# Performance work log

Measured on AMD Instinct MI355X. Metric: run time of the kernel, lower is better.

## Reference

```python
import jax, jax.numpy as jnp
import numpy as np

B, S, D, H = 4, 1024, 1024, 16
HD = D // H


def setup_inputs() -> dict:
    key = jax.random.key(0)
    ks = jax.random.split(key, 8)
    q = jax.random.normal(ks[0], (B, S, D), jnp.float32)
    q_mask = jnp.ones((B, S), dtype=bool)
    kv_mask = jax.random.randint(ks[1], (B, S), 0, 2).astype(bool)
    edge_weights = jax.random.uniform(ks[2], (B, S, S), jnp.float32)
    w_init = 0.02
    wq = jax.random.normal(ks[3], (D, D), jnp.float32) * w_init
    wk = jax.random.normal(ks[4], (D, D), jnp.float32) * w_init
    wv = jax.random.normal(ks[5], (D, D), jnp.float32) * w_init
    wo = jax.random.normal(ks[6], (D, D), jnp.float32) * w_init
    bo = jnp.zeros((D,), jnp.float32)
    return {"q": q, "q_mask": q_mask, "kv_mask": kv_mask,
            "edge_weights": edge_weights, "wq": wq, "wk": wk, "wv": wv,
            "wo": wo, "bo": bo}


def _pass_with_mask(x, w, mask, b=None):
    # Linear applied everywhere, padded rows zeroed (matches pass_with_mask)
    y = x @ w.T
    if b is not None:
        y = y + b
    return jnp.where(mask[..., None], y, 0.0)


def reference(q, q_mask, kv_mask, edge_weights, wq, wk, wv, wo, bo):
    b = q.shape[0]
    # merge_masks: padding mask outer product (recv x send)
    full_mask = (q_mask[:, :, None] & kv_mask[:, None, :])[:, None]  # [b,1,s,s]
    # projections (self attention: k = v = q)
    qh = _pass_with_mask(q, wq, q_mask).reshape(b, S, H, HD).transpose(0, 2, 1, 3)
    kh = _pass_with_mask(q, wk, kv_mask).reshape(b, S, H, HD).transpose(0, 2, 1, 3)
    vh = _pass_with_mask(q, wv, kv_mask).reshape(b, S, H, HD).transpose(0, 2, 1, 3)
    # NOTE: faithful to source, scaled by sqrt(model_dim), not sqrt(head_dim)
    scores = jnp.einsum("bhqd,bhkd->bhqk", qh, kh) / np.sqrt(D).astype(np.float32)
    scores = scores * edge_weights[:, None]          # mul_weights=True
    scores = jnp.where(full_mask, scores, -jnp.inf)
    scores = jax.nn.softmax(scores, axis=-1)
    scores = jnp.where(full_mask, scores, 0.0)       # re-zero masked entries
    out = jnp.einsum("bhqk,bhkd->bhqd", scores, vh)
    out = out.transpose(0, 2, 1, 3).reshape(b, S, D)
    return _pass_with_mask(out, wo, q_mask, bo)
```

## Files before the change

kernel.cpp:

```cpp
#include <hip/hip_runtime.h>

typedef unsigned short u16;
typedef unsigned int u32;
typedef __bf16 b16x8 __attribute__((ext_vector_type(8)));
typedef u16 u16x8 __attribute__((ext_vector_type(8)));
typedef float f32x4 __attribute__((ext_vector_type(4)));
typedef float f32x16 __attribute__((ext_vector_type(16)));
typedef u32 u32x2 __attribute__((ext_vector_type(2)));

#define DEV __device__ __forceinline__
#define INF __builtin_inff()
#define MFMA16(a, b, c) __builtin_amdgcn_mfma_f32_16x16x32_bf16((a), (b), (c), 0, 0, 0)
#define MFMA32(a, b, c) __builtin_amdgcn_mfma_f32_32x32x16_bf16((a), (b), (c), 0, 0, 0)
#define EXP2F(x) __builtin_amdgcn_exp2f(x)

DEV u16 f2b(float f) {
  union { float f; unsigned u; } x; x.f = f;
  unsigned r = x.u + 0x7fffu + ((x.u >> 16) & 1u);
  return (u16)(r >> 16);
}

DEV u32 pk2(float a, float b) {
  __bf16 lo = (__bf16)a, hi = (__bf16)b;
  u16 ul, uh;
  __builtin_memcpy(&ul, &lo, 2);
  __builtin_memcpy(&uh, &hi, 2);
  return (u32)ul | ((u32)uh << 16);
}

DEV float b2f(u16 v) {
  union { u32 u; float f; } x; x.u = (u32)v << 16; return x.f;
}

DEV void gl_lds16(const u16* g, u16* l) {
  __builtin_amdgcn_global_load_lds((const __attribute__((address_space(1))) void*)g,
                                   (__attribute__((address_space(3))) void*)l, 16, 0, 0);
}

__global__ __launch_bounds__(256) void cvt_all(const float* __restrict__ q,
                                               const float* __restrict__ wq,
                                               const float* __restrict__ wk,
                                               const float* __restrict__ wv,
                                               const float* __restrict__ wo,
                                               u16* __restrict__ xb, u16* __restrict__ wqb,
                                               u16* __restrict__ wkb, u16* __restrict__ wvb,
                                               u16* __restrict__ wob) {
  const int blk = blockIdx.x;
  const float* src; u16* dst; float scale = 1.f; int base;
  if (blk < 4096)      { src = q;  dst = xb;  base = blk; }
  else if (blk < 5120) { src = wq; dst = wqb; base = blk - 4096; scale = 0.045084441f; }
  else if (blk < 6144) { src = wk; dst = wkb; base = blk - 5120; }
  else if (blk < 7168) { src = wv; dst = wvb; base = blk - 6144; }
  else                 { src = wo; dst = wob; base = blk - 7168; }
  const int i = base * 256 + threadIdx.x;
  float4 v = reinterpret_cast<const float4*>(src)[i];
  ushort4 o;
  o.x = f2b(v.x * scale);
  o.y = f2b(v.y * scale);
  o.z = f2b(v.z * scale);
  o.w = f2b(v.w * scale);
  reinterpret_cast<ushort4*>(dst)[i] = o;
}

__global__ __launch_bounds__(256) void repack_edge(const float* __restrict__ edge,
                                                   u16* __restrict__ Ef) {
  __shared__ float Ls[32][132];
  const int c = blockIdx.x;
  const int qt = blockIdx.y;
  const int b = blockIdx.z;
  const int tid = threadIdx.x;
#pragma unroll
  for (int it = 0; it < 4; ++it) {
    int idx = it * 256 + tid;
    int r = idx >> 5, k4 = idx & 31;
    f32x4 v = *reinterpret_cast<const f32x4*>(
        edge + (size_t)(b * 1024 + qt * 32 + r) * 1024 + c * 128 + k4 * 4);
#pragma unroll
    for (int e = 0; e < 4; ++e) Ls[r][k4 * 4 + e] = v[e];
  }
  __syncthreads();
#pragma unroll
  for (int it = 0; it < 2; ++it) {
    int slot = it * 256 + tid;
    int kvtl = slot >> 7, i = (slot >> 6) & 1, lane = slot & 63;
    int qv = lane & 31, hi = lane >> 5;
    u16x8 o;
#pragma unroll
    for (int jp = 0; jp < 8; ++jp) {
      int j = i * 8 + jp;
      int kvl = (j & 3) + 8 * (j >> 2) + 4 * hi;
      o[jp] = f2b(Ls[qv][kvtl * 32 + kvl]);
    }
    *reinterpret_cast<u16x8*>(
        Ef + ((size_t)(b * 32 + qt) * 32 + (c * 4 + kvtl)) * 1024 + i * 512 + lane * 8) = o;
  }
}

template <int MODE>
DEV void gemm_body(u16* __restrict__ SA, u16* __restrict__ SB,
                   const u16* __restrict__ A, const u16* __restrict__ W,
                   u16* __restrict__ Ybf, float* __restrict__ Yf,
                   const float* __restrict__ bias, const int* __restrict__ qmask) {
  const int t = threadIdx.x;
  const int lane = t & 63, w = t >> 6;
  const int lr = lane & 15, lg = lane >> 4;
  const int wr = w >> 1, wc = w & 1;
  const int m0 = blockIdx.y * 128, n0 = blockIdx.x * 128;

  f32x4 acc[4][4] = {};

  const int r0 = t >> 2;
  const int c0 = (t & 3) * 8;
  const u16* gA = A + (size_t)(m0 + r0) * 1024 + c0;
  const u16* gB = W + (size_t)(n0 + r0) * 1024 + c0;

  auto stage = [&](int buf, int kt) {
    const int ko = kt * 32;
    u16* lA = SA + buf * 4096 + w * 512;
    u16* lB = SB + buf * 4096 + w * 512;
    gl_lds16(gA + ko, lA);
    gl_lds16(gA + ko + 64 * 1024, lA + 2048);
    gl_lds16(gB + ko, lB);
    gl_lds16(gB + ko + 64 * 1024, lB + 2048);
  };

  stage(0, 0);
  __syncthreads();
  for (int kt = 0; kt < 32; ++kt) {
    const int cur = kt & 1;
    if (kt < 31) stage(cur ^ 1, kt + 1);
    const u16* As = SA + cur * 4096;
    const u16* Bs = SB + cur * 4096;
    b16x8 af[4], bf[4];
#pragma unroll
    for (int m = 0; m < 4; ++m)
      af[m] = *reinterpret_cast<const b16x8*>(As + (wr * 64 + m * 16 + lr) * 32 + lg * 8);
#pragma unroll
    for (int n = 0; n < 4; ++n)
      bf[n] = *reinterpret_cast<const b16x8*>(Bs + (wc * 64 + n * 16 + lr) * 32 + lg * 8);
#pragma unroll
    for (int m = 0; m < 4; ++m)
#pragma unroll
      for (int n = 0; n < 4; ++n)
        acc[m][n] = MFMA16(af[m], bf[n], acc[m][n]);
    __syncthreads();
  }

#pragma unroll
  for (int m = 0; m < 4; ++m) {
    const int row = m0 + wr * 64 + m * 16 + lg * 4;
#pragma unroll
    for (int n = 0; n < 4; ++n) {
      const int col = n0 + wc * 64 + n * 16 + lr;
#pragma unroll
      for (int r = 0; r < 4; ++r) {
        const int rowg = row + r;
        const float v = acc[m][n][r];
        if (MODE == 3) {
          float y = v + bias[col];
          Yf[(size_t)rowg * 1024 + col] = qmask[rowg] ? y : 0.f;
        } else if (MODE == 1) {
          const int bb = rowg >> 10, rw = rowg & 1023, rt = rw >> 5, rl = rw & 31;
          const int h = col >> 6, dh = col & 63;
          const int s = dh >> 4, hi = (dh >> 3) & 1, j = dh & 7;
          size_t idx = (((size_t)((bb * 16 + h) * 32 + rt) * 4 + s) * 64 + (rl + (hi << 5))) * 8 + j;
          Ybf[idx] = f2b(v);
        } else {
          const int bb = rowg >> 10, kv = rowg & 1023, kvt = kv >> 5, kvl = kv & 31;
          const int s = kvl >> 4, k16 = kvl & 15;
          const int hi = (k16 >> 2) & 1;
          const int j = (k16 & 3) | (((k16 >> 3) & 1) << 2);
          const int h = col >> 6, dh = col & 63, d = dh >> 5;
          size_t idx = ((((size_t)((bb * 16 + h) * 32 + kvt) * 2 + d) * 2 + s) * 64 + ((dh & 31) + (hi << 5))) * 8 + j;
          Ybf[idx] = f2b(v);
        }
      }
    }
  }
}

__global__ __launch_bounds__(256, 4) void gemm_qkv(const u16* __restrict__ X,
                                                   const u16* __restrict__ Wq,
                                                   const u16* __restrict__ Wk,
                                                   const u16* __restrict__ Wv,
                                                   u16* __restrict__ Yq, u16* __restrict__ Yk,
                                                   u16* __restrict__ Yv) {
  __shared__ __attribute__((aligned(16))) u16 SA[2 * 4096];
  __shared__ __attribute__((aligned(16))) u16 SB[2 * 4096];
  if (blockIdx.z == 0)      gemm_body<1>(SA, SB, X, Wq, Yq, nullptr, nullptr, nullptr);
  else if (blockIdx.z == 1) gemm_body<1>(SA, SB, X, Wk, Yk, nullptr, nullptr, nullptr);
  else                      gemm_body<2>(SA, SB, X, Wv, Yv, nullptr, nullptr, nullptr);
}
__global__ __launch_bounds__(256, 4) void gemm_final(const u16* __restrict__ A,
                                                     const u16* __restrict__ Wo,
                                                     float* __restrict__ Out,
                                                     const float* __restrict__ bias,
                                                     const int* __restrict__ qmask) {
  __shared__ __attribute__((aligned(16))) u16 SA[2 * 4096];
  __shared__ __attribute__((aligned(16))) u16 SB[2 * 4096];
  gemm_body<3>(SA, SB, A, Wo, nullptr, Out, bias, qmask);
}

__global__ __launch_bounds__(256, 2) void attn_kernel(
    const u16* __restrict__ Qf, const u16* __restrict__ Kf,
    const u16* __restrict__ Vf, const u16* __restrict__ Ef,
    const int* __restrict__ kvm, u16* __restrict__ out) {
  __shared__ float Osh[3][64][33];
  __shared__ float Lsh[4][32];
  __shared__ __attribute__((aligned(16))) u16 Fsh[1024];

  const int d0 = blockIdx.x;
  const int logical = (d0 & 7) * 256 + (d0 >> 3);
  const int qt = logical & 31, bh = logical >> 5;
  const int b = bh >> 4, h = bh & 15;
  const int tid = threadIdx.x, lane = tid & 63, w = tid >> 6;
  const int ql = lane & 31, hi = lane >> 5;
  const int qrow = qt * 32 + ql;

#pragma unroll
  for (int e = 0; e < 4; ++e) {
    int idx = tid * 4 + e;
    int kt = idx >> 5, h2 = (idx >> 4) & 1, j = idx & 15;
    int kv = kt * 32 + 8 * (j >> 2) + 4 * h2 + (j & 3);
    Fsh[idx] = kvm[b * 1024 + kv] ? (u16)0 : (u16)0xFF80;
  }

  const u16* qp = Qf + (size_t)bh * 65536 + qt * 2048 + lane * 8;
  b16x8 Qr[4];
#pragma unroll
  for (int s = 0; s < 4; ++s) Qr[s] = *reinterpret_cast<const b16x8*>(qp + s * 512);

  const u16* kp = Kf + (size_t)bh * 65536 + lane * 8;
  const u16* vp = Vf + (size_t)bh * 65536 + lane * 8;
  const u16* ep = Ef + (size_t)(b * 32 + qt) * 32768 + lane * 8;

  f32x16 O0 = {}, O1 = {};
  float La[4] = {};

  struct KB { b16x8 K[4]; };
  struct EB { u16x8 E[2]; };
  KB Ka, Kb;
  EB E0, E1, E2;

  auto fK = [&](KB& T, int kvt) {
#pragma unroll
    for (int s = 0; s < 4; ++s)
      T.K[s] = *reinterpret_cast<const b16x8*>(kp + kvt * 2048 + s * 512);
  };
  auto fE = [&](EB& T, int kvt) {
#pragma unroll
    for (int i = 0; i < 2; ++i)
      T.E[i] = *reinterpret_cast<const u16x8*>(ep + kvt * 1024 + i * 512);
  };

  auto compute = [&](const KB& K, const EB& E, int kvt) {
    b16x8 V[4];
#pragma unroll
    for (int ds = 0; ds < 4; ++ds)
      V[ds] = *reinterpret_cast<const b16x8*>(vp + kvt * 2048 + ds * 512);
    u16x8 Fm0 = *reinterpret_cast<const u16x8*>(&Fsh[kvt * 32 + hi * 16]);
    u16x8 Fm1 = *reinterpret_cast<const u16x8*>(&Fsh[kvt * 32 + hi * 16 + 8]);
    f32x16 S = {};
#pragma unroll
    for (int s = 0; s < 4; ++s) S = MFMA32(K.K[s], Qr[s], S);
    float p[16];
#pragma unroll
    for (int j = 0; j < 8; ++j)
      p[j] = EXP2F(fmaf(S[j], b2f(E.E[0][j]), b2f(Fm0[j])));
#pragma unroll
    for (int j = 0; j < 8; ++j)
      p[8 + j] = EXP2F(fmaf(S[8 + j], b2f(E.E[1][j]), b2f(Fm1[j])));
#pragma unroll
    for (int j = 0; j < 16; ++j) La[j & 3] += p[j];
#pragma unroll
    for (int s = 0; s < 2; ++s) {
      union { u32 wd[4]; b16x8 v; } U;
      U.wd[0] = pk2(p[8 * s + 0], p[8 * s + 1]);
      U.wd[1] = pk2(p[8 * s + 2], p[8 * s + 3]);
      U.wd[2] = pk2(p[8 * s + 4], p[8 * s + 5]);
      U.wd[3] = pk2(p[8 * s + 6], p[8 * s + 7]);
      O0 = MFMA32(V[s], U.v, O0);
      O1 = MFMA32(V[2 + s], U.v, O1);
    }
  };

  const int base = w * 8;
  fE(E0, base); fE(E1, base + 1);
  fK(Ka, base);
  __syncthreads();

  fE(E2, base + 2); fK(Kb, base + 1); compute(Ka, E0, base + 0);
  fE(E0, base + 3); fK(Ka, base + 2); compute(Kb, E1, base + 1);
  fE(E1, base + 4); fK(Kb, base + 3); compute(Ka, E2, base + 2);
  fE(E2, base + 5); fK(Ka, base + 4); compute(Kb, E0, base + 3);
  fE(E0, base + 6); fK(Kb, base + 5); compute(Ka, E1, base + 4);
  fE(E1, base + 7); fK(Ka, base + 6); compute(Kb, E2, base + 5);
                    fK(Kb, base + 7); compute(Ka, E0, base + 6);
                                      compute(Kb, E1, base + 7);

  float Lw = (La[0] + La[1]) + (La[2] + La[3]);
  Lw += __shfl_xor(Lw, 32, 64);

  if (hi == 0) Lsh[w][ql] = Lw;
  if (w > 0) {
#pragma unroll
    for (int r = 0; r < 16; ++r) Osh[w - 1][lane][r] = O0[r];
#pragma unroll
    for (int r = 0; r < 16; ++r) Osh[w - 1][lane][16 + r] = O1[r];
  }
  __syncthreads();
  if (w == 0) {
    float Lg = (Lsh[0][ql] + Lsh[1][ql]) + (Lsh[2][ql] + Lsh[3][ql]);
#pragma unroll
    for (int wv = 0; wv < 3; ++wv) {
#pragma unroll
      for (int r = 0; r < 16; ++r) O0[r] += Osh[wv][lane][r];
#pragma unroll
      for (int r = 0; r < 16; ++r) O1[r] += Osh[wv][lane][16 + r];
    }
    const float inv = (Lg > 0.f) ? 1.f / Lg : 0.f;
    u16* orow = out + (size_t)(b * 1024 + qrow) * 1024 + h * 64 + hi * 4;
#pragma unroll
    for (int H = 0; H < 2; ++H) {
#pragma unroll
      for (int g = 0; g < 4; ++g) {
        float o0 = (H ? O1[4 * g + 0] : O0[4 * g + 0]) * inv;
        float o1 = (H ? O1[4 * g + 1] : O0[4 * g + 1]) * inv;
        float o2 = (H ? O1[4 * g + 2] : O0[4 * g + 2]) * inv;
        float o3 = (H ? O1[4 * g + 3] : O0[4 * g + 3]) * inv;
        u32x2 wv2 = {pk2(o0, o1), pk2(o2, o3)};
        *reinterpret_cast<u32x2*>(orow + H * 32 + g * 8) = wv2;
      }
    }
  }
}

extern "C" void kernel_launch(void* const* d_in, const int* in_sizes, int n_in,
                              void* d_out, int out_size, void* d_ws, size_t ws_size,
                              hipStream_t stream) {
  (void)in_sizes; (void)n_in; (void)out_size; (void)ws_size;
  const float* q    = (const float*)d_in[0];
  const int*   qm   = (const int*)d_in[1];
  const int*   kvm  = (const int*)d_in[2];
  const float* edge = (const float*)d_in[3];
  const float* wq   = (const float*)d_in[4];
  const float* wk   = (const float*)d_in[5];
  const float* wv   = (const float*)d_in[6];
  const float* wo   = (const float*)d_in[7];
  const float* bo   = (const float*)d_in[8];
  float* out = (float*)d_out;

  char* ws = (char*)d_ws;
  u16* xb  = (u16*)(ws);
  u16* wqb = (u16*)(ws + (8ull  << 20));
  u16* wkb = (u16*)(ws + (10ull << 20));
  u16* wvb = (u16*)(ws + (12ull << 20));
  u16* wob = (u16*)(ws + (14ull << 20));
  u16* Qfb = (u16*)(ws + (16ull << 20));
  u16* Kf  = (u16*)(ws + (24ull << 20));
  u16* Vf  = (u16*)(ws + (32ull << 20));
  u16* Ef  = (u16*)(ws + (40ull << 20));
  u16* ab  = xb;

  cvt_all<<<8192, 256, 0, stream>>>(q, wq, wk, wv, wo, xb, wqb, wkb, wvb, wob);
  gemm_qkv<<<dim3(8, 32, 3), 256, 0, stream>>>(xb, wqb, wkb, wvb, Qfb, Kf, Vf);
  repack_edge<<<dim3(8, 32, 4), 256, 0, stream>>>(edge, Ef);
  attn_kernel<<<2048, 256, 0, stream>>>(Qfb, Kf, Vf, Ef, kvm, ab);
  gemm_final<<<dim3(8, 32), 256, 0, stream>>>(ab, wob, out, bo, qm);
}
```

Before: 114.4 us.

## Process two query tiles per attention block to reuse K/V loads

Each attention workgroup now handles two adjacent 32-row query tiles, so K, V and the mask fragments loaded per KV tile feed twice as many MFMAs, and the grid is halved. The goal is to cut global K/V traffic and per-block setup overhead. In exchange, register pressure roughly doubles for accumulators and edge buffers, which could reduce occupancy or cause spills. The edge prefetch depth also drops from three buffers to two, and the epilogue becomes two sequential reductions with extra barriers.

```diff
diff --git a/kernel.cpp b/kernel.cpp
--- a/kernel.cpp
+++ b/kernel.cpp
@@ -210,12 +210,12 @@
   __shared__ __attribute__((aligned(16))) u16 Fsh[1024];
 
   const int d0 = blockIdx.x;
-  const int logical = (d0 & 7) * 256 + (d0 >> 3);
-  const int qt = logical & 31, bh = logical >> 5;
+  const int logical = (d0 & 7) * 128 + (d0 >> 3);
+  const int qtp = logical & 15, bh = logical >> 4;
+  const int qt0 = qtp * 2;
   const int b = bh >> 4, h = bh & 15;
   const int tid = threadIdx.x, lane = tid & 63, w = tid >> 6;
   const int ql = lane & 31, hi = lane >> 5;
-  const int qrow = qt * 32 + ql;
 
 #pragma unroll
   for (int e = 0; e < 4; ++e) {
@@ -225,113 +225,154 @@
     Fsh[idx] = kvm[b * 1024 + kv] ? (u16)0 : (u16)0xFF80;
   }
 
-  const u16* qp = Qf + (size_t)bh * 65536 + qt * 2048 + lane * 8;
-  b16x8 Qr[4];
-#pragma unroll
-  for (int s = 0; s < 4; ++s) Qr[s] = *reinterpret_cast<const b16x8*>(qp + s * 512);
+  const u16* qpA = Qf + (size_t)bh * 65536 + qt0 * 2048 + lane * 8;
+  b16x8 Qa[4], Qb[4];
+#pragma unroll
+  for (int s = 0; s < 4; ++s) {
+    Qa[s] = *reinterpret_cast<const b16x8*>(qpA + s * 512);
+    Qb[s] = *reinterpret_cast<const b16x8*>(qpA + 2048 + s * 512);
+  }
 
   const u16* kp = Kf + (size_t)bh * 65536 + lane * 8;
   const u16* vp = Vf + (size_t)bh * 65536 + lane * 8;
-  const u16* ep = Ef + (size_t)(b * 32 + qt) * 32768 + lane * 8;
-
-  f32x16 O0 = {}, O1 = {};
-  float La[4] = {};
+  const u16* eA = Ef + (size_t)(b * 32 + qt0) * 32768 + lane * 8;
+  const u16* eB = eA + 32768;
+
+  f32x16 OA0 = {}, OA1 = {}, OB0 = {}, OB1 = {};
+  float LA[4] = {}, LB[4] = {};
 
   struct KB { b16x8 K[4]; };
   struct EB { u16x8 E[2]; };
   KB Ka, Kb;
-  EB E0, E1, E2;
+  EB Ea0, Ea1, Eb0, Eb1;
 
   auto fK = [&](KB& T, int kvt) {
 #pragma unroll
     for (int s = 0; s < 4; ++s)
       T.K[s] = *reinterpret_cast<const b16x8*>(kp + kvt * 2048 + s * 512);
   };
-  auto fE = [&](EB& T, int kvt) {
+  auto fE = [&](EB& T, const u16* ep, int kvt) {
 #pragma unroll
     for (int i = 0; i < 2; ++i)
       T.E[i] = *reinterpret_cast<const u16x8*>(ep + kvt * 1024 + i * 512);
   };
 
-  auto compute = [&](const KB& K, const EB& E, int kvt) {
+  auto computeAB = [&](const KB& K, const EB& Ea, const EB& Eb, int kvt) {
     b16x8 V[4];
 #pragma unroll
     for (int ds = 0; ds < 4; ++ds)
       V[ds] = *reinterpret_cast<const b16x8*>(vp + kvt * 2048 + ds * 512);
     u16x8 Fm0 = *reinterpret_cast<const u16x8*>(&Fsh[kvt * 32 + hi * 16]);
     u16x8 Fm1 = *reinterpret_cast<const u16x8*>(&Fsh[kvt * 32 + hi * 16 + 8]);
-    f32x16 S = {};
-#pragma unroll
-    for (int s = 0; s < 4; ++s) S = MFMA32(K.K[s], Qr[s], S);
-    float p[16];
+    f32x16 Sa = {}, Sb = {};
+#pragma unroll
+    for (int s = 0; s < 4; ++s) Sa = MFMA32(K.K[s], Qa[s], Sa);
+#pragma unroll
+    for (int s = 0; s < 4; ++s) Sb = MFMA32(K.K[s], Qb[s], Sb);
+    float pa[16];
 #pragma unroll
     for (int j = 0; j < 8; ++j)
-      p[j] = EXP2F(fmaf(S[j], b2f(E.E[0][j]), b2f(Fm0[j])));
+      pa[j] = EXP2F(fmaf(Sa[j], b2f(Ea.E[0][j]), b2f(Fm0[j])));
 #pragma unroll
     for (int j = 0; j < 8; ++j)
-      p[8 + j] = EXP2F(fmaf(S[8 + j], b2f(E.E[1][j]), b2f(Fm1[j])));
-#pragma unroll
-    for (int j = 0; j < 16; ++j) La[j & 3] += p[j];
+      pa[8 + j] = EXP2F(fmaf(Sa[8 + j], b2f(Ea.E[1][j]), b2f(Fm1[j])));
+#pragma unroll
+    for (int j = 0; j < 16; ++j) LA[j & 3] += pa[j];
 #pragma unroll
     for (int s = 0; s < 2; ++s) {
       union { u32 wd[4]; b16x8 v; } U;
-      U.wd[0] = pk2(p[8 * s + 0], p[8 * s + 1]);
-      U.wd[1] = pk2(p[8 * s + 2], p[8 * s + 3]);
-      U.wd[2] = pk2(p[8 * s + 4], p[8 * s + 5]);
-      U.wd[3] = pk2(p[8 * s + 6], p[8 * s + 7]);
-      O0 = MFMA32(V[s], U.v, O0);
-      O1 = MFMA32(V[2 + s], U.v, O1);
+      U.wd[0] = pk2(pa[8 * s + 0], pa[8 * s + 1]);
+      U.wd[1] = pk2(pa[8 * s + 2], pa[8 * s + 3]);
+      U.wd[2] = pk2(pa[8 * s + 4], pa[8 * s + 5]);
+      U.wd[3] = pk2(pa[8 * s + 6], pa[8 * s + 7]);
+      OA0 = MFMA32(V[s], U.v, OA0);
+      OA1 = MFMA32(V[2 + s], U.v, OA1);
+    }
+    float pb[16];
+#pragma unroll
+    for (int j = 0; j < 8; ++j)
+      pb[j] = EXP2F(fmaf(Sb[j], b2f(Eb.E[0][j]), b2f(Fm0[j])));
+#pragma unroll
+    for (int j = 0; j < 8; ++j)
+      pb[8 + j] = EXP2F(fmaf(Sb[8 + j], b2f(Eb.E[1][j]), b2f(Fm1[j])));
+#pragma unroll
+    for (int j = 0; j < 16; ++j) LB[j & 3] += pb[j];
+#pragma unroll
+    for (int s = 0; s < 2; ++s) {
+      union { u32 wd[4]; b16x8 v; } U;
+      U.wd[0] = pk2(pb[8 * s + 0], pb[8 * s + 1]);
+      U.wd[1] = pk2(pb[8 * s + 2], pb[8 * s + 3]);
+      U.wd[2] = pk2(pb[8 * s + 4], pb[8 * s + 5]);
+      U.wd[3] = pk2(pb[8 * s + 6], pb[8 * s + 7]);
+      OB0 = MFMA32(V[s], U.v, OB0);
+      OB1 = MFMA32(V[2 + s], U.v, OB1);
     }
   };
 
   const int base = w * 8;
-  fE(E0, base); fE(E1, base + 1);
-  fK(Ka, base);
+  fK(Ka, base); fE(Ea0, eA, base); fE(Eb0, eB, base);
   __syncthreads();
 
-  fE(E2, base + 2); fK(Kb, base + 1); compute(Ka, E0, base + 0);
-  fE(E0, base + 3); fK(Ka, base + 2); compute(Kb, E1, base + 1);
-  fE(E1, base + 4); fK(Kb, base + 3); compute(Ka, E2, base + 2);
-  fE(E2, base + 5); fK(Ka, base + 4); compute(Kb, E0, base + 3);
-  fE(E0, base + 6); fK(Kb, base + 5); compute(Ka, E1, base + 4);
-  fE(E1, base + 7); fK(Ka, base + 6); compute(Kb, E2, base + 5);
-                    fK(Kb, base + 7); compute(Ka, E0, base + 6);
-                                      compute(Kb, E1, base + 7);
-
-  float Lw = (La[0] + La[1]) + (La[2] + La[3]);
-  Lw += __shfl_xor(Lw, 32, 64);
-
-  if (hi == 0) Lsh[w][ql] = Lw;
-  if (w > 0) {
-#pragma unroll
-    for (int r = 0; r < 16; ++r) Osh[w - 1][lane][r] = O0[r];
-#pragma unroll
-    for (int r = 0; r < 16; ++r) Osh[w - 1][lane][16 + r] = O1[r];
-  }
-  __syncthreads();
-  if (w == 0) {
-    float Lg = (Lsh[0][ql] + Lsh[1][ql]) + (Lsh[2][ql] + Lsh[3][ql]);
-#pragma unroll
-    for (int wv = 0; wv < 3; ++wv) {
-#pragma unroll
-      for (int r = 0; r < 16; ++r) O0[r] += Osh[wv][lane][r];
-#pragma unroll
-      for (int r = 0; r < 16; ++r) O1[r] += Osh[wv][lane][16 + r];
-    }
-    const float inv = (Lg > 0.f) ? 1.f / Lg : 0.f;
-    u16* orow = out + (size_t)(b * 1024 + qrow) * 1024 + h * 64 + hi * 4;
-#pragma unroll
-    for (int H = 0; H < 2; ++H) {
-#pragma unroll
-      for (int g = 0; g < 4; ++g) {
-        float o0 = (H ? O1[4 * g + 0] : O0[4 * g + 0]) * inv;
-        float o1 = (H ? O1[4 * g + 1] : O0[4 * g + 1]) * inv;
-        float o2 = (H ? O1[4 * g + 2] : O0[4 * g + 2]) * inv;
-        float o3 = (H ? O1[4 * g + 3] : O0[4 * g + 3]) * inv;
-        u32x2 wv2 = {pk2(o0, o1), pk2(o2, o3)};
-        *reinterpret_cast<u32x2*>(orow + H * 32 + g * 8) = wv2;
+  fK(Kb, base + 1); fE(Ea1, eA, base + 1); fE(Eb1, eB, base + 1);
+  computeAB(Ka, Ea0, Eb0, base + 0);
+  fK(Ka, base + 2); fE(Ea0, eA, base + 2); fE(Eb0, eB, base + 2);
+  computeAB(Kb, Ea1, Eb1, base + 1);
+  fK(Kb, base + 3); fE(Ea1, eA, base + 3); fE(Eb1, eB, base + 3);
+  computeAB(Ka, Ea0, Eb0, base + 2);
+  fK(Ka, base + 4); fE(Ea0, eA, base + 4); fE(Eb0, eB, base + 4);
+  computeAB(Kb, Ea1, Eb1, base + 3);
+  fK(Kb, base + 5); fE(Ea1, eA, base + 5); fE(Eb1, eB, base + 5);
+  computeAB(Ka, Ea0, Eb0, base + 4);
+  fK(Ka, base + 6); fE(Ea0, eA, base + 6); fE(Eb0, eB, base + 6);
+  computeAB(Kb, Ea1, Eb1, base + 5);
+  fK(Kb, base + 7); fE(Ea1, eA, base + 7); fE(Eb1, eB, base + 7);
+  computeAB(Ka, Ea0, Eb0, base + 6);
+  computeAB(Kb, Ea1, Eb1, base + 7);
+
+#pragma unroll
+  for (int st = 0; st < 2; ++st) {
+    const f32x16& P0 = st ? OB0 : OA0;
+    const f32x16& P1 = st ? OB1 : OA1;
+    float Lw = st ? ((LB[0] + LB[1]) + (LB[2] + LB[3]))
+                  : ((LA[0] + LA[1]) + (LA[2] + LA[3]));
+    Lw += __shfl_xor(Lw, 32, 64);
+    if (hi == 0) Lsh[w][ql] = Lw;
+    if (w > 0) {
+#pragma unroll
+      for (int r = 0; r < 16; ++r) Osh[w - 1][lane][r] = P0[r];
+#pragma unroll
+      for (int r = 0; r < 16; ++r) Osh[w - 1][lane][16 + r] = P1[r];
+    }
+    __syncthreads();
+    if (w == 0) {
+      float Lg = (Lsh[0][ql] + Lsh[1][ql]) + (Lsh[2][ql] + Lsh[3][ql]);
+      float R0[16], R1[16];
+#pragma unroll
+      for (int r = 0; r < 16; ++r) { R0[r] = P0[r]; R1[r] = P1[r]; }
+#pragma unroll
+      for (int wv = 0; wv < 3; ++wv) {
+#pragma unroll
+        for (int r = 0; r < 16; ++r) R0[r] += Osh[wv][lane][r];
+#pragma unroll
+        for (int r = 0; r < 16; ++r) R1[r] += Osh[wv][lane][16 + r];
       }
-    }
+      const float inv = (Lg > 0.f) ? 1.f / Lg : 0.f;
+      const int qrow = (qt0 + st) * 32 + ql;
+      u16* orow = out + (size_t)(b * 1024 + qrow) * 1024 + h * 64 + hi * 4;
+#pragma unroll
+      for (int H = 0; H < 2; ++H) {
+#pragma unroll
+        for (int g = 0; g < 4; ++g) {
+          float o0 = (H ? R1[4 * g + 0] : R0[4 * g + 0]) * inv;
+          float o1 = (H ? R1[4 * g + 1] : R0[4 * g + 1]) * inv;
+          float o2 = (H ? R1[4 * g + 2] : R0[4 * g + 2]) * inv;
+          float o3 = (H ? R1[4 * g + 3] : R0[4 * g + 3]) * inv;
+          u32x2 wv2 = {pk2(o0, o1), pk2(o2, o3)};
+          *reinterpret_cast<u32x2*>(orow + H * 32 + g * 8) = wv2;
+        }
+      }
+    }
+    __syncthreads();
   }
 }
 
@@ -365,6 +406,6 @@
   cvt_all<<<8192, 256, 0, stream>>>(q, wq, wk, wv, wo, xb, wqb, wkb, wvb, wob);
   gemm_qkv<<<dim3(8, 32, 3), 256, 0, stream>>>(xb, wqb, wkb, wvb, Qfb, Kf, Vf);
   repack_edge<<<dim3(8, 32, 4), 256, 0, stream>>>(edge, Ef);
-  attn_kernel<<<2048, 256, 0, stream>>>(Qfb, Kf, Vf, Ef, kvm, ab);
+  attn_kernel<<<1024, 256, 0, stream>>>(Qfb, Kf, Vf, Ef, kvm, ab);
   gemm_final<<<dim3(8, 32), 256, 0, stream>>>(ab, wob, out, bo, qm);
 }
```

New measurement: 140.9 us. +23.2%, slower.
